# Optimization experiments

Hardware: AMD Instinct MI355X
Metric: run time of the kernel (lower is better)

The kernel has to match this reference:

```python
import jax, jax.numpy as jnp
import numpy as np

B, S, H, D = 4, 8192, 8, 64  # batch, seq, heads, head_dim
M = 64                        # num random features
EPS = 1e-6


def setup_inputs() -> dict:
    key = jax.random.key(0)
    k1, k2, k3, k4 = jax.random.split(key, 4)
    qs = jax.random.normal(k1, (B, S, H, D), dtype=jnp.float32)
    ks = jax.random.normal(k2, (B, S, H, D), dtype=jnp.float32)
    vs = jax.random.normal(k3, (B, S, H, D), dtype=jnp.float32)
    proj = jax.random.normal(k4, (M, D), dtype=jnp.float32)
    return {"qs": qs, "ks": ks, "vs": vs, "proj": proj}


def _phi(x, proj):
    # stable positive softmax kernel: exp(x @ proj^T - ||x||^2/2) / sqrt(m)
    m = proj.shape[0]
    x_proj = jnp.einsum('...d,md->...m', x, proj)
    h = jnp.sum(jnp.square(x), axis=-1, keepdims=True) * 0.5
    return jnp.exp(x_proj - h) / jnp.sqrt(jnp.asarray(m, x.dtype))


def reference(qs, ks, vs, proj):
    Bq, Q, Hh, Dqk = qs.shape
    K = ks.shape[1]
    Dv = vs.shape[-1]
    # (B, S, H, D) -> (B*H, S, D)
    q = qs.transpose(0, 2, 1, 3).reshape(-1, Q, Dqk)
    k = ks.transpose(0, 2, 1, 3).reshape(-1, K, Dqk)
    v = vs.transpose(0, 2, 1, 3).reshape(-1, K, Dv)
    normalizer = 1.0 / jnp.power(jnp.asarray(Dqk, q.dtype), 0.25)
    q_prime = _phi(q * normalizer, proj)  # (B*H, Q, M)
    k_prime = _phi(k * normalizer, proj)  # (B*H, K, M)
    # fast_attend: linear-time attention
    c = jnp.concatenate([v, jnp.ones((*v.shape[:-1], 1), v.dtype)], axis=-1)  # (B*H, K, Dv+1)
    buf1 = jnp.einsum('bkm,bkc->bmc', k_prime, c)   # (B*H, M, Dv+1)
    buf2 = jnp.einsum('bqm,bmc->bqc', q_prime, buf1)  # (B*H, Q, Dv+1)
    num, den = buf2[..., :-1], buf2[..., -1]
    den = jnp.where(den < EPS, EPS, den)
    ctx = num / den[..., None]
    return ctx.reshape(Bq, Hh, Q, Dv).transpose(0, 2, 1, 3)
```

## Files before the change

kernel.cpp:

```cpp
#include <hip/hip_runtime.h>

#define S_ 8192
#define H_ 8
#define D_ 64
#define M_ 64
#define BH_ 32
#define CPK_ 80
#define NCHK 16
#define NCHQ 16
#define TILE 64
#define KTILES (S_ / NCHK / TILE)
#define QTILES (S_ / NCHQ / TILE)

typedef short bf16x8 __attribute__((ext_vector_type(8)));
typedef float f32x4 __attribute__((ext_vector_type(4)));

constexpr float XS_ = 0.35355339059327373f * 1.4426950408889634f;
constexpr float HS_ = 0.34657359027997264f;
constexpr float EPS_ = 1e-6f;

__device__ __forceinline__ unsigned short f2bf(float f) {
    unsigned int u = __float_as_uint(f);
    u += 0x7FFFu + ((u >> 16) & 1u);
    return (unsigned short)(u >> 16);
}
__device__ __forceinline__ float fexp2(float x) { return __builtin_amdgcn_exp2f(x); }

#define MFMA(a, b, c) __builtin_amdgcn_mfma_f32_16x16x32_bf16((a), (b), (c), 0, 0, 0)
#define SWZ(byteoff, row) ((byteoff) ^ (((row) & 7) << 4))

__global__ void __launch_bounds__(256)
fa_k(const float* __restrict__ ks, const float* __restrict__ vs,
     const float* __restrict__ proj, float* __restrict__ partial)
{
    const int chunk = blockIdx.x;
    const int bh    = blockIdx.y;
    const int b = bh >> 3, h = bh & 7;
    const int tid = threadIdx.x, wid = tid >> 6, lane = tid & 63;
    const int l15 = lane & 15, g = lane >> 4;

    __shared__ __align__(16) char eTb[2][M_ * TILE * 2];
    __shared__ __align__(16) char vTb[2][D_ * TILE * 2];

    const int rows = S_ / NCHK;
    const int s0 = chunk * rows;
    const size_t rs = (size_t)H_ * D_;
    const float* kb = ks + ((size_t)b * S_ * H_ + h) * D_;
    const float* vb = vs + ((size_t)b * S_ * H_ + h) * D_;

    bf16x8 pf[4][2];
#pragma unroll
    for (int mt = 0; mt < 4; ++mt)
#pragma unroll
        for (int kk = 0; kk < 2; ++kk) {
            const float* p = proj + (mt * 16 + l15) * D_ + kk * 32 + g * 8;
            float4 a = *(const float4*)p, c = *(const float4*)(p + 4);
            bf16x8 f;
            f[0] = (short)f2bf(a.x); f[1] = (short)f2bf(a.y);
            f[2] = (short)f2bf(a.z); f[3] = (short)f2bf(a.w);
            f[4] = (short)f2bf(c.x); f[5] = (short)f2bf(c.y);
            f[6] = (short)f2bf(c.z); f[7] = (short)f2bf(c.w);
            pf[mt][kk] = f;
        }

    bf16x8 onef = {0, 0, 0, 0, 0, 0, 0, 0};
    if (l15 == 0) {
#pragma unroll
        for (int j = 0; j < 8; ++j) onef[j] = (short)0x3F80;
    }

    f32x4 acc[5];
#pragma unroll
    for (int ci = 0; ci < 5; ++ci) acc[ci] = (f32x4){0.f, 0.f, 0.f, 0.f};

    auto loadT = [&](int t, float4* kp, float* vp) {
        int sb = s0 + t * TILE;
        const float* krow = kb + (size_t)(sb + wid * 16 + l15) * rs;
        kp[0] = *(const float4*)(krow + g * 8);
        kp[1] = *(const float4*)(krow + g * 8 + 4);
        kp[2] = *(const float4*)(krow + 32 + g * 8);
        kp[3] = *(const float4*)(krow + 32 + g * 8 + 4);
        const float* vcol = vb + lane;
        int rb = sb + wid * 16;
#pragma unroll
        for (int r = 0; r < 16; ++r)
            vp[r] = vcol[(size_t)(rb + r) * rs];
    };

    auto body = [&](int t, int p, const float4* kc, const float* vc,
                    float4* kn, float* vn) {
        if (t + 1 < KTILES) loadT(t + 1, kn, vn);

        float kx[16];
#pragma unroll
        for (int i = 0; i < 4; ++i) {
            kx[4 * i + 0] = kc[i].x * XS_; kx[4 * i + 1] = kc[i].y * XS_;
            kx[4 * i + 2] = kc[i].z * XS_; kx[4 * i + 3] = kc[i].w * XS_;
        }
        float sq = 0.f;
#pragma unroll
        for (int j = 0; j < 16; ++j) sq += kx[j] * kx[j];
        sq += __shfl_xor(sq, 16);
        sq += __shfl_xor(sq, 32);
        float hrow = sq * HS_ + 3.0f;

        bf16x8 a1[2];
#pragma unroll
        for (int j = 0; j < 8; ++j) {
            a1[0][j] = (short)f2bf(kx[j]);
            a1[1][j] = (short)f2bf(kx[8 + j]);
        }

        f32x4 pa[4];
#pragma unroll
        for (int mt = 0; mt < 4; ++mt) {
            pa[mt] = (f32x4){0.f, 0.f, 0.f, 0.f};
            pa[mt] = MFMA(a1[0], pf[mt][0], pa[mt]);
            pa[mt] = MFMA(a1[1], pf[mt][1], pa[mt]);
        }

        float hr[4];
#pragma unroll
        for (int r = 0; r < 4; ++r) hr[r] = __shfl(hrow, 4 * g + r);

        char* etp = eTb[p];
        char* vtp = vTb[p];
#pragma unroll
        for (int mt = 0; mt < 4; ++mt) {
            unsigned long long pk = 0;
#pragma unroll
            for (int r = 0; r < 4; ++r) {
                float e = fexp2(pa[mt][r] - hr[r]);
                pk |= (unsigned long long)f2bf(e) << (16 * r);
            }
            int m = mt * 16 + l15;
            *(unsigned long long*)(etp + SWZ(m * 128 + 32 * wid + 8 * g, m)) = pk;
        }
        {
            int c = lane;
            bf16x8 w0, w1;
#pragma unroll
            for (int j = 0; j < 8; ++j) {
                w0[j] = (short)f2bf(vc[j]);
                w1[j] = (short)f2bf(vc[8 + j]);
            }
            *(bf16x8*)(vtp + SWZ(c * 128 + 32 * wid, c)) = w0;
            *(bf16x8*)(vtp + SWZ(c * 128 + 32 * wid + 16, c)) = w1;
        }
        __syncthreads();

        bf16x8 a2[2];
        {
            int m = wid * 16 + l15;
            a2[0] = *(const bf16x8*)(etp + SWZ(m * 128 + 16 * g, m));
            a2[1] = *(const bf16x8*)(etp + SWZ(m * 128 + 16 * g + 64, m));
        }
#pragma unroll
        for (int ci = 0; ci < 4; ++ci) {
            int c = ci * 16 + l15;
            bf16x8 b0 = *(const bf16x8*)(vtp + SWZ(c * 128 + 16 * g, c));
            bf16x8 b1 = *(const bf16x8*)(vtp + SWZ(c * 128 + 16 * g + 64, c));
            acc[ci] = MFMA(a2[0], b0, acc[ci]);
            acc[ci] = MFMA(a2[1], b1, acc[ci]);
        }
        acc[4] = MFMA(a2[0], onef, acc[4]);
        acc[4] = MFMA(a2[1], onef, acc[4]);
    };

    float4 ka[4], kb2[4];
    float va[16], vb2[16];
    loadT(0, ka, va);
    for (int t = 0; t < KTILES; t += 2) {
        body(t, 0, ka, va, kb2, vb2);
        body(t + 1, 1, kb2, vb2, ka, va);
    }

    float* dst = partial + ((size_t)bh * NCHK + chunk) * (M_ * CPK_);
#pragma unroll
    for (int ci = 0; ci < 5; ++ci)
#pragma unroll
        for (int r = 0; r < 4; ++r)
            dst[(wid * 16 + 4 * g + r) * CPK_ + ci * 16 + l15] = acc[ci][r];
}

__global__ void __launch_bounds__(256)
fa_r(const float* __restrict__ partial, float* __restrict__ buf1)
{
    int e = blockIdx.x * 256 + threadIdx.x;
    if (e >= BH_ * M_ * CPK_) return;
    int bh = e / (M_ * CPK_);
    int r  = e - bh * (M_ * CPK_);
    const float* src = partial + (size_t)bh * NCHK * (M_ * CPK_) + r;
    float s0 = 0.f, s1 = 0.f, s2 = 0.f, s3 = 0.f;
#pragma unroll
    for (int ch = 0; ch < NCHK; ch += 4) {
        s0 += src[(size_t)(ch + 0) * (M_ * CPK_)];
        s1 += src[(size_t)(ch + 1) * (M_ * CPK_)];
        s2 += src[(size_t)(ch + 2) * (M_ * CPK_)];
        s3 += src[(size_t)(ch + 3) * (M_ * CPK_)];
    }
    buf1[e] = (s0 + s1) + (s2 + s3);
}

__global__ void __launch_bounds__(256)
fa_q(const float* __restrict__ qs, const float* __restrict__ proj,
     const float* __restrict__ buf1, float* __restrict__ out)
{
    const int chunk = blockIdx.x;
    const int bh    = blockIdx.y;
    const int b = bh >> 3, h = bh & 7;
    const int tid = threadIdx.x, wid = tid >> 6, lane = tid & 63;
    const int l15 = lane & 15, g = lane >> 4;

    __shared__ __align__(16) char eLb[2][TILE * M_ * 2];
    __shared__ __align__(16) char b1tb[CPK_ * M_ * 2];

    const int rows = S_ / NCHQ;
    const int s0 = chunk * rows;
    const size_t rs = (size_t)H_ * D_;
    const float* qb = qs + ((size_t)b * S_ * H_ + h) * D_;

    const float* b1 = buf1 + (size_t)bh * (M_ * CPK_);
    for (int i = tid; i < M_ * CPK_; i += 256) {
        int m = i / CPK_, c = i - m * CPK_;
        *(unsigned short*)(b1tb + SWZ(c * 128 + 2 * m, c)) = f2bf(b1[i]);
    }

    bf16x8 pf[4][2];
#pragma unroll
    for (int mt = 0; mt < 4; ++mt)
#pragma unroll
        for (int kk = 0; kk < 2; ++kk) {
            const float* p = proj + (mt * 16 + l15) * D_ + kk * 32 + g * 8;
            float4 a = *(const float4*)p, c = *(const float4*)(p + 4);
            bf16x8 f;
            f[0] = (short)f2bf(a.x); f[1] = (short)f2bf(a.y);
            f[2] = (short)f2bf(a.z); f[3] = (short)f2bf(a.w);
            f[4] = (short)f2bf(c.x); f[5] = (short)f2bf(c.y);
            f[6] = (short)f2bf(c.z); f[7] = (short)f2bf(c.w);
            pf[mt][kk] = f;
        }
    __syncthreads();

    bf16x8 af3[5][2];
#pragma unroll
    for (int ci = 0; ci < 5; ++ci)
#pragma unroll
        for (int kk = 0; kk < 2; ++kk) {
            int c = ci * 16 + l15;
            af3[ci][kk] = *(const bf16x8*)(b1tb + SWZ(c * 128 + 16 * g + 64 * kk, c));
        }

    auto loadQ = [&](int t, float4* qp) {
        int sb = s0 + t * TILE;
        const float* qrow = qb + (size_t)(sb + wid * 16 + l15) * rs;
        qp[0] = *(const float4*)(qrow + g * 8);
        qp[1] = *(const float4*)(qrow + g * 8 + 4);
        qp[2] = *(const float4*)(qrow + 32 + g * 8);
        qp[3] = *(const float4*)(qrow + 32 + g * 8 + 4);
    };

    auto body = [&](int t, int p, const float4* qc, float4* qn) {
        if (t + 1 < QTILES) loadQ(t + 1, qn);

        float kx[16];
#pragma unroll
        for (int i = 0; i < 4; ++i) {
            kx[4 * i + 0] = qc[i].x * XS_; kx[4 * i + 1] = qc[i].y * XS_;
            kx[4 * i + 2] = qc[i].z * XS_; kx[4 * i + 3] = qc[i].w * XS_;
        }
        float sq = 0.f;
#pragma unroll
        for (int j = 0; j < 16; ++j) sq += kx[j] * kx[j];
        sq += __shfl_xor(sq, 16);
        sq += __shfl_xor(sq, 32);
        float hrow = sq * HS_ + 3.0f;

        bf16x8 a1[2];
#pragma unroll
        for (int j = 0; j < 8; ++j) {
            a1[0][j] = (short)f2bf(kx[j]);
            a1[1][j] = (short)f2bf(kx[8 + j]);
        }

        f32x4 pa[4];
#pragma unroll
        for (int mt = 0; mt < 4; ++mt) {
            pa[mt] = (f32x4){0.f, 0.f, 0.f, 0.f};
            pa[mt] = MFMA(a1[0], pf[mt][0], pa[mt]);
            pa[mt] = MFMA(a1[1], pf[mt][1], pa[mt]);
        }

        float hr[4];
#pragma unroll
        for (int r = 0; r < 4; ++r) hr[r] = __shfl(hrow, 4 * g + r);

        char* elp = eLb[p];
#pragma unroll
        for (int mt = 0; mt < 4; ++mt) {
            int m = mt * 16 + l15;
#pragma unroll
            for (int r = 0; r < 4; ++r) {
                float e = fexp2(pa[mt][r] - hr[r]);
                int qrow = wid * 16 + 4 * g + r;
                *(unsigned short*)(elp + SWZ(qrow * 128 + 2 * m, qrow)) = f2bf(e);
            }
        }
        __syncthreads();

        bf16x8 b3[2];
        {
            int qrow = wid * 16 + l15;
            b3[0] = *(const bf16x8*)(elp + SWZ(qrow * 128 + 16 * g, qrow));
            b3[1] = *(const bf16x8*)(elp + SWZ(qrow * 128 + 16 * g + 64, qrow));
        }
        f32x4 dt[5];
#pragma unroll
        for (int ci = 0; ci < 5; ++ci) {
            dt[ci] = (f32x4){0.f, 0.f, 0.f, 0.f};
            dt[ci] = MFMA(af3[ci][0], b3[0], dt[ci]);
            dt[ci] = MFMA(af3[ci][1], b3[1], dt[ci]);
        }

        float den = __shfl(dt[4][0], l15);
        float rd = 1.0f / fmaxf(den, EPS_);

        int sg = s0 + t * TILE + wid * 16 + l15;
        size_t base = (((size_t)b * S_ + sg) * H_ + h) * D_;
#pragma unroll
        for (int ci = 0; ci < 4; ++ci) {
            f32x4 o;
#pragma unroll
            for (int r = 0; r < 4; ++r) o[r] = dt[ci][r] * rd;
            *(f32x4*)(out + base + ci * 16 + 4 * g) = o;
        }
    };

    float4 qa[4], qb2[4];
    loadQ(0, qa);
    for (int t = 0; t < QTILES; t += 2) {
        body(t, 0, qa, qb2);
        body(t + 1, 1, qb2, qa);
    }
}

extern "C" void kernel_launch(void* const* d_in, const int* in_sizes, int n_in,
                              void* d_out, int out_size, void* d_ws, size_t ws_size,
                              hipStream_t stream)
{
    const float* qs   = (const float*)d_in[0];
    const float* ks   = (const float*)d_in[1];
    const float* vs   = (const float*)d_in[2];
    const float* proj = (const float*)d_in[3];
    float* out = (float*)d_out;

    float* partial = (float*)d_ws;
    float* buf1 = partial + (size_t)BH_ * NCHK * (M_ * CPK_);

    fa_k<<<dim3(NCHK, BH_), 256, 0, stream>>>(ks, vs, proj, partial);
    int nred = (BH_ * M_ * CPK_ + 255) / 256;
    fa_r<<<dim3(nred), 256, 0, stream>>>(partial, buf1);
    fa_q<<<dim3(NCHQ, BH_), 256, 0, stream>>>(qs, proj, buf1, out);
}
```

Baseline: 72.83 us.

## Split K-side reduction into more chunks and use packed bf16 conversions

The K/V pass now picks its chunk count at runtime, preferring 32 chunks per head when the workspace is large enough. This doubles the number of blocks for better occupancy across CUs, at the cost of more partial sums for the reduce kernel. Scalar float-to-bf16 rounding is also replaced with the packed two-element bf16 conversion intrinsic, which cuts per-element conversion ALU work in both the K and Q passes. The runtime loop bounds also give up some compile-time unrolling.

```diff
diff --git a/kernel.cpp b/kernel.cpp
--- a/kernel.cpp
+++ b/kernel.cpp
@@ -1,4 +1,5 @@
 #include <hip/hip_runtime.h>
+#include <hip/hip_bf16.h>
 
 #define S_ 8192
 #define H_ 8
@@ -6,10 +7,8 @@
 #define M_ 64
 #define BH_ 32
 #define CPK_ 80
-#define NCHK 16
 #define NCHQ 16
 #define TILE 64
-#define KTILES (S_ / NCHK / TILE)
 #define QTILES (S_ / NCHQ / TILE)
 
 typedef short bf16x8 __attribute__((ext_vector_type(8)));
@@ -24,6 +23,10 @@
     u += 0x7FFFu + ((u >> 16) & 1u);
     return (unsigned short)(u >> 16);
 }
+__device__ __forceinline__ unsigned int pkbf(float lo, float hi) {
+    __hip_bfloat162 t = __float22bfloat162_rn(float2{lo, hi});
+    return *reinterpret_cast<unsigned int*>(&t);
+}
 __device__ __forceinline__ float fexp2(float x) { return __builtin_amdgcn_exp2f(x); }
 
 #define MFMA(a, b, c) __builtin_amdgcn_mfma_f32_16x16x32_bf16((a), (b), (c), 0, 0, 0)
@@ -31,7 +34,8 @@
 
 __global__ void __launch_bounds__(256)
 fa_k(const float* __restrict__ ks, const float* __restrict__ vs,
-     const float* __restrict__ proj, float* __restrict__ partial)
+     const float* __restrict__ proj, float* __restrict__ partial,
+     int nch, int ktiles)
 {
     const int chunk = blockIdx.x;
     const int bh    = blockIdx.y;
@@ -42,7 +46,7 @@
     __shared__ __align__(16) char eTb[2][M_ * TILE * 2];
     __shared__ __align__(16) char vTb[2][D_ * TILE * 2];
 
-    const int rows = S_ / NCHK;
+    const int rows = ktiles * TILE;
     const int s0 = chunk * rows;
     const size_t rs = (size_t)H_ * D_;
     const float* kb = ks + ((size_t)b * S_ * H_ + h) * D_;
@@ -89,7 +93,7 @@
 
     auto body = [&](int t, int p, const float4* kc, const float* vc,
                     float4* kn, float* vn) {
-        if (t + 1 < KTILES) loadT(t + 1, kn, vn);
+        if (t + 1 < ktiles) loadT(t + 1, kn, vn);
 
         float kx[16];
 #pragma unroll
@@ -104,19 +108,19 @@
         sq += __shfl_xor(sq, 32);
         float hrow = sq * HS_ + 3.0f;
 
-        bf16x8 a1[2];
-#pragma unroll
-        for (int j = 0; j < 8; ++j) {
-            a1[0][j] = (short)f2bf(kx[j]);
-            a1[1][j] = (short)f2bf(kx[8 + j]);
+        union { bf16x8 v; unsigned int u[4]; } A0, A1;
+#pragma unroll
+        for (int i = 0; i < 4; ++i) {
+            A0.u[i] = pkbf(kx[2 * i], kx[2 * i + 1]);
+            A1.u[i] = pkbf(kx[8 + 2 * i], kx[9 + 2 * i]);
         }
 
         f32x4 pa[4];
 #pragma unroll
         for (int mt = 0; mt < 4; ++mt) {
             pa[mt] = (f32x4){0.f, 0.f, 0.f, 0.f};
-            pa[mt] = MFMA(a1[0], pf[mt][0], pa[mt]);
-            pa[mt] = MFMA(a1[1], pf[mt][1], pa[mt]);
+            pa[mt] = MFMA(A0.v, pf[mt][0], pa[mt]);
+            pa[mt] = MFMA(A1.v, pf[mt][1], pa[mt]);
         }
 
         float hr[4];
@@ -127,25 +131,25 @@
         char* vtp = vTb[p];
 #pragma unroll
         for (int mt = 0; mt < 4; ++mt) {
-            unsigned long long pk = 0;
-#pragma unroll
-            for (int r = 0; r < 4; ++r) {
-                float e = fexp2(pa[mt][r] - hr[r]);
-                pk |= (unsigned long long)f2bf(e) << (16 * r);
-            }
+            float e0 = fexp2(pa[mt][0] - hr[0]);
+            float e1 = fexp2(pa[mt][1] - hr[1]);
+            float e2 = fexp2(pa[mt][2] - hr[2]);
+            float e3 = fexp2(pa[mt][3] - hr[3]);
+            unsigned long long pk = (unsigned long long)pkbf(e0, e1)
+                                  | ((unsigned long long)pkbf(e2, e3) << 32);
             int m = mt * 16 + l15;
             *(unsigned long long*)(etp + SWZ(m * 128 + 32 * wid + 8 * g, m)) = pk;
         }
         {
             int c = lane;
-            bf16x8 w0, w1;
-#pragma unroll
-            for (int j = 0; j < 8; ++j) {
-                w0[j] = (short)f2bf(vc[j]);
-                w1[j] = (short)f2bf(vc[8 + j]);
+            union { bf16x8 v; unsigned int u[4]; } W0, W1;
+#pragma unroll
+            for (int i = 0; i < 4; ++i) {
+                W0.u[i] = pkbf(vc[2 * i], vc[2 * i + 1]);
+                W1.u[i] = pkbf(vc[8 + 2 * i], vc[9 + 2 * i]);
             }
-            *(bf16x8*)(vtp + SWZ(c * 128 + 32 * wid, c)) = w0;
-            *(bf16x8*)(vtp + SWZ(c * 128 + 32 * wid + 16, c)) = w1;
+            *(bf16x8*)(vtp + SWZ(c * 128 + 32 * wid, c)) = W0.v;
+            *(bf16x8*)(vtp + SWZ(c * 128 + 32 * wid + 16, c)) = W1.v;
         }
         __syncthreads();
 
@@ -170,12 +174,12 @@
     float4 ka[4], kb2[4];
     float va[16], vb2[16];
     loadT(0, ka, va);
-    for (int t = 0; t < KTILES; t += 2) {
+    for (int t = 0; t + 2 <= ktiles; t += 2) {
         body(t, 0, ka, va, kb2, vb2);
         body(t + 1, 1, kb2, vb2, ka, va);
     }
 
-    float* dst = partial + ((size_t)bh * NCHK + chunk) * (M_ * CPK_);
+    float* dst = partial + ((size_t)bh * nch + chunk) * (M_ * CPK_);
 #pragma unroll
     for (int ci = 0; ci < 5; ++ci)
 #pragma unroll
@@ -184,21 +188,22 @@
 }
 
 __global__ void __launch_bounds__(256)
-fa_r(const float* __restrict__ partial, float* __restrict__ buf1)
+fa_r(const float* __restrict__ partial, float* __restrict__ buf1, int nch)
 {
     int e = blockIdx.x * 256 + threadIdx.x;
     if (e >= BH_ * M_ * CPK_) return;
     int bh = e / (M_ * CPK_);
     int r  = e - bh * (M_ * CPK_);
-    const float* src = partial + (size_t)bh * NCHK * (M_ * CPK_) + r;
+    const float* src = partial + (size_t)bh * nch * (M_ * CPK_) + r;
     float s0 = 0.f, s1 = 0.f, s2 = 0.f, s3 = 0.f;
-#pragma unroll
-    for (int ch = 0; ch < NCHK; ch += 4) {
+    int ch = 0;
+    for (; ch + 4 <= nch; ch += 4) {
         s0 += src[(size_t)(ch + 0) * (M_ * CPK_)];
         s1 += src[(size_t)(ch + 1) * (M_ * CPK_)];
         s2 += src[(size_t)(ch + 2) * (M_ * CPK_)];
         s3 += src[(size_t)(ch + 3) * (M_ * CPK_)];
     }
+    for (; ch < nch; ++ch) s0 += src[(size_t)ch * (M_ * CPK_)];
     buf1[e] = (s0 + s1) + (s2 + s3);
 }
 
@@ -276,19 +281,19 @@
         sq += __shfl_xor(sq, 32);
         float hrow = sq * HS_ + 3.0f;
 
-        bf16x8 a1[2];
-#pragma unroll
-        for (int j = 0; j < 8; ++j) {
-            a1[0][j] = (short)f2bf(kx[j]);
-            a1[1][j] = (short)f2bf(kx[8 + j]);
+        union { bf16x8 v; unsigned int u[4]; } A0, A1;
+#pragma unroll
+        for (int i = 0; i < 4; ++i) {
+            A0.u[i] = pkbf(kx[2 * i], kx[2 * i + 1]);
+            A1.u[i] = pkbf(kx[8 + 2 * i], kx[9 + 2 * i]);
         }
 
         f32x4 pa[4];
 #pragma unroll
         for (int mt = 0; mt < 4; ++mt) {
             pa[mt] = (f32x4){0.f, 0.f, 0.f, 0.f};
-            pa[mt] = MFMA(a1[0], pf[mt][0], pa[mt]);
-            pa[mt] = MFMA(a1[1], pf[mt][1], pa[mt]);
+            pa[mt] = MFMA(A0.v, pf[mt][0], pa[mt]);
+            pa[mt] = MFMA(A1.v, pf[mt][1], pa[mt]);
         }
 
         float hr[4];
@@ -354,11 +359,17 @@
     const float* proj = (const float*)d_in[3];
     float* out = (float*)d_out;
 
+    int nch = 32;
+    while (nch > 16 &&
+           (size_t)BH_ * (size_t)(nch + 1) * (M_ * CPK_) * sizeof(float) > ws_size)
+        nch >>= 1;
+    int ktiles = S_ / nch / TILE;
+
     float* partial = (float*)d_ws;
-    float* buf1 = partial + (size_t)BH_ * NCHK * (M_ * CPK_);
-
-    fa_k<<<dim3(NCHK, BH_), 256, 0, stream>>>(ks, vs, proj, partial);
+    float* buf1 = partial + (size_t)BH_ * nch * (M_ * CPK_);
+
+    fa_k<<<dim3(nch, BH_), 256, 0, stream>>>(ks, vs, proj, partial, nch, ktiles);
     int nred = (BH_ * M_ * CPK_ + 255) / 256;
-    fa_r<<<dim3(nred), 256, 0, stream>>>(partial, buf1);
+    fa_r<<<dim3(nred), 256, 0, stream>>>(partial, buf1, nch);
     fa_q<<<dim3(NCHQ, BH_), 256, 0, stream>>>(qs, proj, buf1, out);
 }
```

After: 77.97 us. 1.07x slower.
